# Kernel optimization log

Measured on AMD Instinct MI355X. Metric: run time of the kernel, lower is better.

Reference implementation:

```python
import jax, jax.numpy as jnp
import numpy as np
import math

VOCAB = 390
D = 512
D_INNER = 2048
H = 8
DH = D // H
L = 6
MAX_SEQ = 1024
BATCH = 4
OUT = 2
PAD = 0
EPS = 1e-6


def sinusoid(max_seq, d):
    pos = np.arange(max_seq, dtype=np.float64)[:, None]
    i = np.arange(d, dtype=np.float64)[None, :]
    angle = (pos * np.exp(-np.log(10000.0) * i / d) * np.exp(np.log(10000.0) / d * (i % 2))
             + 0.5 * np.pi * (i % 2))
    return np.sin(angle)[None].astype(np.float32)  # [1, max_seq, d]


def setup_inputs() -> dict:
    key = jax.random.key(0)
    ks = jax.random.split(key, 16)
    s = 0.02
    emb = jax.random.uniform(ks[0], (VOCAB, D), jnp.float32, -0.1, 0.1)
    emb = emb.at[PAD].set(0.0)  # padding_idx row zeroed
    inp = {
        'x': jax.random.randint(ks[1], (BATCH, MAX_SEQ), 0, VOCAB, dtype=jnp.int64) if jax.config.jax_enable_x64 else jax.random.randint(ks[1], (BATCH, MAX_SEQ), 0, VOCAB, dtype=jnp.int32),
        'emb': emb,
        'pos': jnp.asarray(sinusoid(MAX_SEQ, D)),
        'Wq': jax.random.normal(ks[2], (L, D, D), jnp.float32) * s,
        'bq': jnp.zeros((L, D), jnp.float32),
        'Wk': jax.random.normal(ks[3], (L, D, D), jnp.float32) * s,
        'bk': jnp.zeros((L, D), jnp.float32),
        'Wv': jax.random.normal(ks[4], (L, D, D), jnp.float32) * s,
        'bv': jnp.zeros((L, D), jnp.float32),
        'Wo': jax.random.normal(ks[5], (L, D, D), jnp.float32) * s,
        'bo': jnp.zeros((L, D), jnp.float32),
        'E': jax.random.normal(ks[6], (L, MAX_SEQ, DH), jnp.float32),
        'W1': jax.random.normal(ks[7], (L, D, D_INNER), jnp.float32) * s,
        'b1': jnp.zeros((L, D_INNER), jnp.float32),
        'W2': jax.random.normal(ks[8], (L, D_INNER, D), jnp.float32) * s,
        'b2': jnp.zeros((L, D), jnp.float32),
        'ln1_s': jnp.ones((L, D), jnp.float32),
        'ln1_b': jnp.zeros((L, D), jnp.float32),
        'ln2_s': jnp.ones((L, D), jnp.float32),
        'ln2_b': jnp.zeros((L, D), jnp.float32),
        'Wf': jax.random.normal(ks[9], (D, OUT), jnp.float32) * s,
        'bf': jnp.zeros((OUT,), jnp.float32),
    }
    return inp


def _layernorm(x, scale, bias):
    mu = jnp.mean(x, axis=-1, keepdims=True)
    var = jnp.mean(jnp.square(x - mu), axis=-1, keepdims=True)
    return (x - mu) * jax.lax.rsqrt(var + EPS) * scale + bias


def _rel_attention(x, Wq, bq, Wk, bk, Wv, bv, Wo, bo, E):
    b, s, d = x.shape
    q = (x @ Wq + bq).reshape(b, s, H, DH).transpose(0, 2, 1, 3)  # [b,h,s,dh]
    k = (x @ Wk + bk).reshape(b, s, H, DH).transpose(0, 2, 1, 3)
    v = (x @ Wv + bv).reshape(b, s, H, DH).transpose(0, 2, 1, 3)
    m = MAX_SEQ  # len_q == len_k == max_seq -> full E
    QE = jnp.einsum('bhld,md->bhlm', q, E)  # [b,h,s,m]
    # qe masking: keep position j >= m-1-i for query row i
    keep = (jnp.arange(m)[None, :] >= (m - 1 - jnp.arange(s))[:, None]).astype(QE.dtype)
    QE = QE * keep
    # skewing trick: pad-left on last dim, reshape, drop first row
    padded = jnp.pad(QE, ((0, 0), (0, 0), (0, 0), (1, 0)))  # [b,h,s,m+1]
    Srel = padded.reshape(b, H, m + 1, s)[:, :, 1:, :]  # [b,h,m,s] == [b,h,s,s]
    logits = (jnp.einsum('bhqd,bhkd->bhqk', q, k) + Srel) / math.sqrt(DH)
    attn = jax.nn.softmax(logits, axis=-1)
    out = jnp.einsum('bhqk,bhkd->bhqd', attn, v)
    out = out.transpose(0, 2, 1, 3).reshape(b, s, d)
    return out @ Wo + bo


def reference(x, emb, pos, Wq, bq, Wk, bk, Wv, bv, Wo, bo, E, W1, b1, W2, b2,
              ln1_s, ln1_b, ln2_s, ln2_b, Wf, bf):
    h = emb[x] * math.sqrt(D)  # [b,s,d]
    h = h + pos[:, :h.shape[1], :]
    for i in range(L):
        attn = _rel_attention(h, Wq[i], bq[i], Wk[i], bk[i], Wv[i], bv[i], Wo[i], bo[i], E[i])
        h1 = _layernorm(attn + h, ln1_s[i], ln1_b[i])
        ffn = jax.nn.relu(h1 @ W1[i] + b1[i]) @ W2[i] + b2[i]
        h = _layernorm(h1 + ffn, ln2_s[i], ln2_b[i])
    return jnp.tanh(h[:, 0, :] @ Wf + bf)  # [b, OUT]
```

## Files before the change

### kernel.cpp

```cpp
#include <hip/hip_runtime.h>
#include <math.h>

#define BATCH  4
#define SEQ    1024
#define DM     512
#define DI     2048
#define NH     8
#define DH     64
#define NL     6
#define NOUT   2

typedef unsigned short u16;
typedef short s16x8 __attribute__((ext_vector_type(8)));
typedef float f32x4 __attribute__((ext_vector_type(4)));
typedef unsigned short u16x4 __attribute__((ext_vector_type(4)));

#define MFMA16(a, b, c) __builtin_amdgcn_mfma_f32_16x16x32_bf16((a), (b), (c), 0, 0, 0)

static constexpr float SQRT_D = 22.627416997969522f;

__device__ __forceinline__ u16 f2b(float x) {
    union { float f; unsigned u; } v; v.f = x;
    unsigned r = v.u + 0x7fffu + ((v.u >> 16) & 1u);
    return (u16)(r >> 16);
}
__device__ __forceinline__ float b2f(u16 b) {
    union { unsigned u; float f; } v; v.u = ((unsigned)b) << 16; return v.f;
}

__global__ __launch_bounds__(256) void k_embed(const int* __restrict__ x,
                                               const float* __restrict__ emb,
                                               const float* __restrict__ pos,
                                               float* __restrict__ h,
                                               u16* __restrict__ hb) {
    const int idx = blockIdx.x * 256 + threadIdx.x;
    const int d4  = idx & 127;
    const int bs  = idx >> 7;
    const int s   = bs & (SEQ - 1);
    const int tok = x[bs];
    const float4 e = ((const float4*)emb)[tok * 128 + d4];
    const float4 p = ((const float4*)pos)[s * 128 + d4];
    float4 r;
    r.x = e.x * SQRT_D + p.x;  r.y = e.y * SQRT_D + p.y;
    r.z = e.z * SQRT_D + p.z;  r.w = e.w * SQRT_D + p.w;
    ((float4*)h)[idx] = r;
    u16x4 rb = { f2b(r.x), f2b(r.y), f2b(r.z), f2b(r.w) };
    ((u16x4*)hb)[idx] = rb;
}

__global__ __launch_bounds__(256) void k_conv(const float* __restrict__ Wq, const float* __restrict__ Wk,
                                              const float* __restrict__ Wv, const float* __restrict__ Wo,
                                              const float* __restrict__ W1, const float* __restrict__ W2,
                                              const float* __restrict__ E,
                                              u16* __restrict__ Wqkvt, u16* __restrict__ Wot,
                                              u16* __restrict__ W1t,  u16* __restrict__ W2t,
                                              u16* __restrict__ Ebf, int layer) {
    const int tb = blockIdx.x;
    if (tb >= 3072) {
        const int rem = tb - 3072;
        const int idx = rem * 1024 + threadIdx.x * 4;
        const float4 v = *(const float4*)(E + (size_t)layer * SEQ * DH + idx);
        u16x4 o = { f2b(v.x), f2b(v.y), f2b(v.z), f2b(v.w) };
        *(u16x4*)(Ebf + idx) = o;
        return;
    }
    __shared__ float T[32][33];
    const float* src; u16* dst; int Ksz, Nsz, tk, tn;
    if (tb < 768) {
        const int mat = tb >> 8, rem = tb & 255;
        src = (mat == 0 ? Wq : (mat == 1 ? Wk : Wv)) + (size_t)layer * DM * DM;
        dst = Wqkvt + (size_t)mat * DM * DM;
        Ksz = 512; Nsz = 512; tk = rem & 15; tn = rem >> 4;
    } else if (tb < 1024) {
        const int rem = tb - 768;
        src = Wo + (size_t)layer * DM * DM; dst = Wot;
        Ksz = 512; Nsz = 512; tk = rem & 15; tn = rem >> 4;
    } else if (tb < 2048) {
        const int rem = tb - 1024;
        src = W1 + (size_t)layer * DM * DI; dst = W1t;
        Ksz = 512; Nsz = 2048; tk = rem & 15; tn = rem >> 4;
    } else {
        const int rem = tb - 2048;
        src = W2 + (size_t)layer * DI * DM; dst = W2t;
        Ksz = 2048; Nsz = 512; tk = rem >> 4; tn = rem & 15;
    }
    {
        const int rr = threadIdx.x >> 3, c4 = (threadIdx.x & 7) << 2;
        const float4 v = *(const float4*)(src + (size_t)(tk * 32 + rr) * Nsz + tn * 32 + c4);
        T[rr][c4 + 0] = v.x; T[rr][c4 + 1] = v.y; T[rr][c4 + 2] = v.z; T[rr][c4 + 3] = v.w;
    }
    __syncthreads();
    {
        const int nl = threadIdx.x >> 3, k4 = (threadIdx.x & 7) << 2;
        u16x4 o = { f2b(T[k4 + 0][nl]), f2b(T[k4 + 1][nl]), f2b(T[k4 + 2][nl]), f2b(T[k4 + 3][nl]) };
        *(u16x4*)(dst + (size_t)(tn * 32 + nl) * Ksz + tk * 32 + k4) = o;
    }
}

template <int RELU, int WRITE_BF16>
__global__ __launch_bounds__(256) void k_mm(const u16* __restrict__ A,
                                            const u16* __restrict__ Bt,
                                            const float* __restrict__ bias0,
                                            const float* __restrict__ bias1,
                                            const float* __restrict__ bias2,
                                            float* __restrict__ Cf,
                                            u16* __restrict__ Cb,
                                            int K, int ldc, int seg_shift, size_t seg_stride) {
    __shared__ u16 As[128 * 40];
    __shared__ u16 Bs[128 * 40];

    const int n0 = blockIdx.x << 7;
    const int m0 = blockIdx.y << 7;
    const int t  = threadIdx.x;
    const int lane = t & 63, w = t >> 6;
    const int n16 = lane & 15, quad = lane >> 4;
    const int wr = (w & 1) << 6;
    const int wc = (w >> 1) << 6;

    const f32x4 z = {0.f, 0.f, 0.f, 0.f};
    f32x4 acc[4][4];
#pragma unroll
    for (int i = 0; i < 4; ++i)
#pragma unroll
        for (int j = 0; j < 4; ++j) acc[i][j] = z;

    const int sr = t >> 2, sk = (t & 3) << 3;
    const u16* Ag = A  + (size_t)(m0 + sr) * K + sk;
    const u16* Bg = Bt + (size_t)(n0 + sr) * K + sk;

    for (int k0 = 0; k0 < K; k0 += 32) {
        __syncthreads();
        *(uint4*)&As[sr * 40 + sk]        = *(const uint4*)(Ag + k0);
        *(uint4*)&As[(sr + 64) * 40 + sk] = *(const uint4*)(Ag + (size_t)64 * K + k0);
        *(uint4*)&Bs[sr * 40 + sk]        = *(const uint4*)(Bg + k0);
        *(uint4*)&Bs[(sr + 64) * 40 + sk] = *(const uint4*)(Bg + (size_t)64 * K + k0);
        __syncthreads();

        s16x8 af[4], bfr[4];
#pragma unroll
        for (int rb = 0; rb < 4; ++rb)
            af[rb] = *(const s16x8*)&As[(wr + rb * 16 + n16) * 40 + quad * 8];
#pragma unroll
        for (int cb = 0; cb < 4; ++cb)
            bfr[cb] = *(const s16x8*)&Bs[(wc + cb * 16 + n16) * 40 + quad * 8];
#pragma unroll
        for (int rb = 0; rb < 4; ++rb)
#pragma unroll
            for (int cb = 0; cb < 4; ++cb)
                acc[rb][cb] = MFMA16(af[rb], bfr[cb], acc[rb][cb]);
    }

    const int sel = n0 >> seg_shift;
    const int colbase = (n0 & ((1 << seg_shift) - 1)) + wc;
    const float* bias = (sel == 0) ? bias0 : (sel == 1 ? bias1 : bias2);
    const size_t cbase = (size_t)sel * seg_stride;

#pragma unroll
    for (int cb = 0; cb < 4; ++cb) {
        const int col = colbase + cb * 16 + n16;
        const float bv = bias[col];
#pragma unroll
        for (int rb = 0; rb < 4; ++rb) {
#pragma unroll
            for (int rr = 0; rr < 4; ++rr) {
                const int row = m0 + wr + rb * 16 + quad * 4 + rr;
                float v = acc[rb][cb][rr] + bv;
                if (RELU) v = fmaxf(v, 0.f);
                const size_t idx = cbase + (size_t)row * ldc + col;
                if (WRITE_BF16) Cb[idx] = f2b(v);
                else            Cf[idx] = v;
            }
        }
    }
}

__global__ __launch_bounds__(256) void k_attn(const u16* __restrict__ Qg,
                                              const u16* __restrict__ Kg,
                                              const u16* __restrict__ Vg,
                                              const u16* __restrict__ Eg,
                                              u16* __restrict__ Og) {
    __shared__ u16 Qs[64 * 72];
    __shared__ u16 Ks[64 * 72];
    __shared__ u16 Vts[64 * 72];
    __shared__ u16 Ps[64 * 72];
    __shared__ float arena[64 * 128];
    u16* Es = (u16*)arena;

    const int i0 = blockIdx.x << 6;
    const int hd = blockIdx.y;
    const int b  = blockIdx.z;
    const int t  = threadIdx.x;
    const int lane = t & 63;
    const int n16 = lane & 15;
    const int quad = lane >> 4;
    const int w = t >> 6;
    const int rw = w << 4;

    const size_t gb = (size_t)b * SEQ * DM + hd * DH;

    {
        int c = t, r = c >> 3, k8 = (c & 7) << 3;
        *(uint4*)&Qs[r * 72 + k8] = *(const uint4*)(Qg + gb + (size_t)(i0 + r) * DM + k8);
        c = t + 256; r = c >> 3; k8 = (c & 7) << 3;
        *(uint4*)&Qs[r * 72 + k8] = *(const uint4*)(Qg + gb + (size_t)(i0 + r) * DM + k8);
    }

    const f32x4 z = {0.f, 0.f, 0.f, 0.f};
    f32x4 Oa[4] = {z, z, z, z};
    float m_run[4] = {-1e30f, -1e30f, -1e30f, -1e30f};
    float l_run[4] = {0.f, 0.f, 0.f, 0.f};

    for (int ct = 0; ct < 16; ++ct) {
        const int c0 = ct << 6;
        const bool active = (c0 <= i0);

        __syncthreads();
        {
            int c = t, r = c >> 3, k8 = (c & 7) << 3;
            *(uint4*)&Ks[r * 72 + k8] = *(const uint4*)(Kg + gb + (size_t)(c0 + r) * DM + k8);
            c = t + 256; r = c >> 3; k8 = (c & 7) << 3;
            *(uint4*)&Ks[r * 72 + k8] = *(const uint4*)(Kg + gb + (size_t)(c0 + r) * DM + k8);
        }
        {
            int c = t, j = c >> 3, d8 = (c & 7) << 3;
            uint4 v = *(const uint4*)(Vg + gb + (size_t)(c0 + j) * DM + d8);
            const u16* pv = (const u16*)&v;
#pragma unroll
            for (int e = 0; e < 8; ++e) Vts[(d8 + e) * 72 + j] = pv[e];
            c = t + 256; j = c >> 3; d8 = (c & 7) << 3;
            v = *(const uint4*)(Vg + gb + (size_t)(c0 + j) * DM + d8);
            const u16* pv2 = (const u16*)&v;
#pragma unroll
            for (int e = 0; e < 8; ++e) Vts[(d8 + e) * 72 + j] = pv2[e];
        }
        if (active) {
            const int eb = 960 - i0 + c0;
#pragma unroll
            for (int p = 0; p < 4; ++p) {
                const int c = t + (p << 8);
                const int u = c >> 3, k8 = (c & 7) << 3;
                int m = eb + u; m = m > 1023 ? 1023 : m;
                *(uint4*)&Es[u * 72 + k8] = *(const uint4*)(Eg + (size_t)m * DH + k8);
            }
        }
        __syncthreads();

        const s16x8 qa0 = *(const s16x8*)&Qs[(rw + n16) * 72 + quad * 8];
        const s16x8 qa1 = *(const s16x8*)&Qs[(rw + n16) * 72 + quad * 8 + 32];

        f32x4 S[4] = {z, z, z, z};
#pragma unroll
        for (int cb = 0; cb < 4; ++cb) {
            const s16x8 k0 = *(const s16x8*)&Ks[(cb * 16 + n16) * 72 + quad * 8];
            const s16x8 k1 = *(const s16x8*)&Ks[(cb * 16 + n16) * 72 + quad * 8 + 32];
            S[cb] = MFMA16(qa0, k0, S[cb]);
            S[cb] = MFMA16(qa1, k1, S[cb]);
        }

        if (active) {
            f32x4 qe[8];
#pragma unroll
            for (int ub = 0; ub < 8; ++ub) qe[ub] = z;
#pragma unroll
            for (int ub = 0; ub < 8; ++ub) {
                const s16x8 e0 = *(const s16x8*)&Es[(ub * 16 + n16) * 72 + quad * 8];
                const s16x8 e1 = *(const s16x8*)&Es[(ub * 16 + n16) * 72 + quad * 8 + 32];
                qe[ub] = MFMA16(qa0, e0, qe[ub]);
                qe[ub] = MFMA16(qa1, e1, qe[ub]);
            }
            __syncthreads();
#pragma unroll
            for (int ub = 0; ub < 8; ++ub)
#pragma unroll
                for (int rr = 0; rr < 4; ++rr)
                    arena[(rw + quad * 4 + rr) * 128 + ub * 16 + n16] = qe[ub][rr];
            const int dqc = i0 - c0;
#pragma unroll
            for (int cb = 0; cb < 4; ++cb)
#pragma unroll
                for (int rr = 0; rr < 4; ++rr) {
                    const int ir = rw + quad * 4 + rr;
                    const int d = cb * 16 + n16 - ir;
                    const float srel = (d <= dqc) ? arena[ir * 128 + 63 + d] : 0.f;
                    S[cb][rr] = (S[cb][rr] + srel) * 0.125f;
                }
        } else {
#pragma unroll
            for (int cb = 0; cb < 4; ++cb)
#pragma unroll
                for (int rr = 0; rr < 4; ++rr) S[cb][rr] *= 0.125f;
        }

        float mt[4], al[4], rs[4], p[4][4];
#pragma unroll
        for (int rr = 0; rr < 4; ++rr)
            mt[rr] = fmaxf(fmaxf(S[0][rr], S[1][rr]), fmaxf(S[2][rr], S[3][rr]));
#pragma unroll
        for (int rr = 0; rr < 4; ++rr) {
            mt[rr] = fmaxf(mt[rr], __shfl_xor(mt[rr], 1, 64));
            mt[rr] = fmaxf(mt[rr], __shfl_xor(mt[rr], 2, 64));
            mt[rr] = fmaxf(mt[rr], __shfl_xor(mt[rr], 4, 64));
            mt[rr] = fmaxf(mt[rr], __shfl_xor(mt[rr], 8, 64));
        }
#pragma unroll
        for (int rr = 0; rr < 4; ++rr) {
            const float mn = fmaxf(m_run[rr], mt[rr]);
            al[rr] = __expf(m_run[rr] - mn);
            m_run[rr] = mn;
        }
#pragma unroll
        for (int cb = 0; cb < 4; ++cb)
#pragma unroll
            for (int rr = 0; rr < 4; ++rr) p[cb][rr] = __expf(S[cb][rr] - m_run[rr]);
#pragma unroll
        for (int rr = 0; rr < 4; ++rr) {
            rs[rr] = p[0][rr] + p[1][rr] + p[2][rr] + p[3][rr];
            rs[rr] += __shfl_xor(rs[rr], 1, 64);
            rs[rr] += __shfl_xor(rs[rr], 2, 64);
            rs[rr] += __shfl_xor(rs[rr], 4, 64);
            rs[rr] += __shfl_xor(rs[rr], 8, 64);
            l_run[rr] = l_run[rr] * al[rr] + rs[rr];
        }
#pragma unroll
        for (int db = 0; db < 4; ++db)
#pragma unroll
            for (int rr = 0; rr < 4; ++rr) Oa[db][rr] *= al[rr];
#pragma unroll
        for (int cb = 0; cb < 4; ++cb)
#pragma unroll
            for (int rr = 0; rr < 4; ++rr)
                Ps[(rw + quad * 4 + rr) * 72 + cb * 16 + n16] = f2b(p[cb][rr]);

        const s16x8 pa0 = *(const s16x8*)&Ps[(rw + n16) * 72 + quad * 8];
        const s16x8 pa1 = *(const s16x8*)&Ps[(rw + n16) * 72 + quad * 8 + 32];
#pragma unroll
        for (int db = 0; db < 4; ++db) {
            const s16x8 v0 = *(const s16x8*)&Vts[(db * 16 + n16) * 72 + quad * 8];
            const s16x8 v1 = *(const s16x8*)&Vts[(db * 16 + n16) * 72 + quad * 8 + 32];
            Oa[db] = MFMA16(pa0, v0, Oa[db]);
            Oa[db] = MFMA16(pa1, v1, Oa[db]);
        }
    }

    float inv[4];
#pragma unroll
    for (int rr = 0; rr < 4; ++rr) inv[rr] = 1.f / l_run[rr];
#pragma unroll
    for (int db = 0; db < 4; ++db)
#pragma unroll
        for (int rr = 0; rr < 4; ++rr) {
            const int row = i0 + rw + quad * 4 + rr;
            Og[gb + (size_t)row * DM + db * 16 + n16] = f2b(Oa[db][rr] * inv[rr]);
        }
}

__global__ __launch_bounds__(128) void k_ln(const float* __restrict__ A,
                                            const float* __restrict__ R,
                                            const float* __restrict__ sc,
                                            const float* __restrict__ bi,
                                            float* __restrict__ Y,
                                            u16* __restrict__ Yb) {
    const int r = blockIdx.x, t = threadIdx.x;
    const float4 a = ((const float4*)(A + (size_t)r * DM))[t];
    const float4 b = ((const float4*)(R + (size_t)r * DM))[t];
    float4 v;
    v.x = a.x + b.x; v.y = a.y + b.y; v.z = a.z + b.z; v.w = a.w + b.w;

    float s = v.x + v.y + v.z + v.w;
#pragma unroll
    for (int o = 32; o > 0; o >>= 1) s += __shfl_down(s, o, 64);
    __shared__ float r1[2], r2[2];
    if ((t & 63) == 0) r1[t >> 6] = s;
    __syncthreads();
    const float mean = (r1[0] + r1[1]) * (1.f / 512.f);

    float4 d;
    d.x = v.x - mean; d.y = v.y - mean; d.z = v.z - mean; d.w = v.w - mean;
    float q = d.x * d.x + d.y * d.y + d.z * d.z + d.w * d.w;
#pragma unroll
    for (int o = 32; o > 0; o >>= 1) q += __shfl_down(q, o, 64);
    if ((t & 63) == 0) r2[t >> 6] = q;
    __syncthreads();
    const float rsq = rsqrtf((r2[0] + r2[1]) * (1.f / 512.f) + 1e-6f);

    const float4 s4 = ((const float4*)sc)[t];
    const float4 b4 = ((const float4*)bi)[t];
    float4 y;
    y.x = d.x * rsq * s4.x + b4.x;
    y.y = d.y * rsq * s4.y + b4.y;
    y.z = d.z * rsq * s4.z + b4.z;
    y.w = d.w * rsq * s4.w + b4.w;
    ((float4*)(Y + (size_t)r * DM))[t] = y;
    u16x4 yb = { f2b(y.x), f2b(y.y), f2b(y.z), f2b(y.w) };
    ((u16x4*)(Yb + (size_t)r * DM))[t] = yb;
}

__global__ __launch_bounds__(512) void k_head(const float* __restrict__ h,
                                              const float* __restrict__ Wf,
                                              const float* __restrict__ bf,
                                              float* __restrict__ out) {
    const int t = threadIdx.x;
    const int w = t >> 6, lane = t & 63;
    const int b = w >> 1, oo = w & 1;
    float s = 0.f;
    for (int d = lane; d < DM; d += 64)
        s += h[(size_t)b * SEQ * DM + d] * Wf[d * NOUT + oo];
#pragma unroll
    for (int o = 32; o > 0; o >>= 1) s += __shfl_down(s, o, 64);
    if (lane == 0) out[b * NOUT + oo] = tanhf(s + bf[oo]);
}

extern "C" void kernel_launch(void* const* d_in, const int* in_sizes, int n_in,
                              void* d_out, int out_size, void* d_ws, size_t ws_size,
                              hipStream_t stream) {
    const int*   x    = (const int*)d_in[0];
    const float* emb  = (const float*)d_in[1];
    const float* pos  = (const float*)d_in[2];
    const float* Wq   = (const float*)d_in[3];
    const float* bq   = (const float*)d_in[4];
    const float* Wk   = (const float*)d_in[5];
    const float* bk   = (const float*)d_in[6];
    const float* Wv   = (const float*)d_in[7];
    const float* bv   = (const float*)d_in[8];
    const float* Wo   = (const float*)d_in[9];
    const float* bo   = (const float*)d_in[10];
    const float* E    = (const float*)d_in[11];
    const float* W1   = (const float*)d_in[12];
    const float* b1   = (const float*)d_in[13];
    const float* W2   = (const float*)d_in[14];
    const float* b2   = (const float*)d_in[15];
    const float* ln1s = (const float*)d_in[16];
    const float* ln1b = (const float*)d_in[17];
    const float* ln2s = (const float*)d_in[18];
    const float* ln2b = (const float*)d_in[19];
    const float* Wf   = (const float*)d_in[20];
    const float* bfp  = (const float*)d_in[21];
    float* out = (float*)d_out;

    char* W = (char*)d_ws;
    float* h    = (float*)(W);
    float* h1   = (float*)(W + (8u  << 20));
    u16*   hb   = (u16*)  (W + (16u << 20));
    u16*   h1b  = (u16*)  (W + (20u << 20));
    u16*   qb   = (u16*)  (W + (24u << 20));
    u16*   kb   = (u16*)  (W + (28u << 20));
    u16*   vb   = (u16*)  (W + (32u << 20));
    u16*   tb   = (u16*)  (W + (36u << 20));
    u16*   midb = qb;
    u16*   Wqkvt= (u16*)  (W + (40u << 20));
    u16*   Wot  = (u16*)  (W + (40u << 20) + 1572864);
    u16*   W1t  = (u16*)  (W + (42u << 20));
    u16*   W2t  = (u16*)  (W + (44u << 20));
    u16*   Ebf  = (u16*)  (W + (46u << 20));

    const int M = BATCH * SEQ;
    const size_t SEG = (size_t)M * DM;

    k_embed<<<(BATCH * SEQ * DM / 4) / 256, 256, 0, stream>>>(x, emb, pos, h, hb);

    for (int l = 0; l < NL; ++l) {
        k_conv<<<3136, 256, 0, stream>>>(Wq, Wk, Wv, Wo, W1, W2, E,
                                         Wqkvt, Wot, W1t, W2t, Ebf, l);
        k_mm<0, 1><<<dim3(12, 32), 256, 0, stream>>>(hb, Wqkvt,
            bq + l * DM, bk + l * DM, bv + l * DM, nullptr, qb, 512, 512, 9, SEG);
        k_attn<<<dim3(16, 8, 4), 256, 0, stream>>>(qb, kb, vb, Ebf, tb);
        k_mm<0, 0><<<dim3(4, 32), 256, 0, stream>>>(tb, Wot,
            bo + l * DM, bo + l * DM, bo + l * DM, h1, nullptr, 512, 512, 30, 0);
        k_ln<<<M, 128, 0, stream>>>(h1, h, ln1s + l * DM, ln1b + l * DM, h1, h1b);
        k_mm<1, 1><<<dim3(16, 32), 256, 0, stream>>>(h1b, W1t,
            b1 + l * DI, b1 + l * DI, b1 + l * DI, nullptr, midb, 512, 2048, 30, 0);
        k_mm<0, 0><<<dim3(4, 32), 256, 0, stream>>>(midb, W2t,
            b2 + l * DM, b2 + l * DM, b2 + l * DM, h, nullptr, 2048, 512, 30, 0);
        k_ln<<<M, 128, 0, stream>>>(h, h1, ln2s + l * DM, ln2b + l * DM, h, hb);
    }

    k_head<<<1, 512, 0, stream>>>(h, Wf, bfp, out);
}
```

Measured before the change: 1.248 ms.

## Batch weight conversion, write V transposed from GEMM, restructure attention and LayerNorm

```diff
diff --git a/kernel.cpp b/kernel.cpp
--- a/kernel.cpp
+++ b/kernel.cpp
@@ -18,6 +18,12 @@
 #define MFMA16(a, b, c) __builtin_amdgcn_mfma_f32_16x16x32_bf16((a), (b), (c), 0, 0, 0)
 
 static constexpr float SQRT_D = 22.627416997969522f;
+
+#define SLOT_WO   786432
+#define SLOT_W1   1048576
+#define SLOT_W2   2097152
+#define SLOT_E    3145728
+#define SLOT_SZ   3211264
 
 __device__ __forceinline__ u16 f2b(float x) {
     union { float f; unsigned u; } v; v.f = x;
@@ -52,10 +58,16 @@
                                               const float* __restrict__ Wv, const float* __restrict__ Wo,
                                               const float* __restrict__ W1, const float* __restrict__ W2,
                                               const float* __restrict__ E,
-                                              u16* __restrict__ Wqkvt, u16* __restrict__ Wot,
-                                              u16* __restrict__ W1t,  u16* __restrict__ W2t,
-                                              u16* __restrict__ Ebf, int layer) {
-    const int tb = blockIdx.x;
+                                              u16* __restrict__ wbase, int layer0, int slot_stride) {
+    const int ll = blockIdx.x / 3136;
+    const int tb = blockIdx.x - ll * 3136;
+    const int layer = layer0 + ll;
+    u16* Wqkvt = wbase + (size_t)ll * slot_stride;
+    u16* Wot   = Wqkvt + SLOT_WO;
+    u16* W1t   = Wqkvt + SLOT_W1;
+    u16* W2t   = Wqkvt + SLOT_W2;
+    u16* Ebf   = Wqkvt + SLOT_E;
+
     if (tb >= 3072) {
         const int rem = tb - 3072;
         const int idx = rem * 1024 + threadIdx.x * 4;
@@ -97,7 +109,7 @@
     }
 }
 
-template <int RELU, int WRITE_BF16>
+template <int RELU, int WRITE_BF16, int SEGV>
 __global__ __launch_bounds__(256) void k_mm(const u16* __restrict__ A,
                                             const u16* __restrict__ Bt,
                                             const float* __restrict__ bias0,
@@ -105,6 +117,7 @@
                                             const float* __restrict__ bias2,
                                             float* __restrict__ Cf,
                                             u16* __restrict__ Cb,
+                                            u16* __restrict__ Vt,
                                             int K, int ldc, int seg_shift, size_t seg_stride) {
     __shared__ u16 As[128 * 40];
     __shared__ u16 Bs[128 * 40];
@@ -166,9 +179,15 @@
                 const int row = m0 + wr + rb * 16 + quad * 4 + rr;
                 float v = acc[rb][cb][rr] + bv;
                 if (RELU) v = fmaxf(v, 0.f);
-                const size_t idx = cbase + (size_t)row * ldc + col;
-                if (WRITE_BF16) Cb[idx] = f2b(v);
-                else            Cf[idx] = v;
+                if (SEGV && sel == 2) {
+                    const size_t vi = (((size_t)(row >> 10) * NH + (col >> 6)) * DH + (col & 63))
+                                      * SEQ + (row & (SEQ - 1));
+                    Vt[vi] = f2b(v);
+                } else if (WRITE_BF16) {
+                    Cb[cbase + (size_t)row * ldc + col] = f2b(v);
+                } else {
+                    Cf[cbase + (size_t)row * ldc + col] = v;
+                }
             }
         }
     }
@@ -176,15 +195,11 @@
 
 __global__ __launch_bounds__(256) void k_attn(const u16* __restrict__ Qg,
                                               const u16* __restrict__ Kg,
-                                              const u16* __restrict__ Vg,
+                                              const u16* __restrict__ Vt,
                                               const u16* __restrict__ Eg,
                                               u16* __restrict__ Og) {
-    __shared__ u16 Qs[64 * 72];
-    __shared__ u16 Ks[64 * 72];
-    __shared__ u16 Vts[64 * 72];
+    __shared__ u16 arena[128 * 72];
     __shared__ u16 Ps[64 * 72];
-    __shared__ float arena[64 * 128];
-    u16* Es = (u16*)arena;
 
     const int i0 = blockIdx.x << 6;
     const int hd = blockIdx.y;
@@ -193,95 +208,65 @@
     const int lane = t & 63;
     const int n16 = lane & 15;
     const int quad = lane >> 4;
-    const int w = t >> 6;
-    const int rw = w << 4;
-
-    const size_t gb = (size_t)b * SEQ * DM + hd * DH;
-
-    {
-        int c = t, r = c >> 3, k8 = (c & 7) << 3;
-        *(uint4*)&Qs[r * 72 + k8] = *(const uint4*)(Qg + gb + (size_t)(i0 + r) * DM + k8);
-        c = t + 256; r = c >> 3; k8 = (c & 7) << 3;
-        *(uint4*)&Qs[r * 72 + k8] = *(const uint4*)(Qg + gb + (size_t)(i0 + r) * DM + k8);
-    }
+    const int rw = (t >> 6) << 4;
+    const int ir_base = rw + (quad << 2);
+
+    const size_t gb  = (size_t)b * SEQ * DM + hd * DH;
+    const size_t vtb = ((size_t)b * NH + hd) * DH * SEQ;
+
+    const u16* qp = Qg + gb + (size_t)(i0 + rw + n16) * DM + quad * 8;
+    const s16x8 qa0 = *(const s16x8*)qp;
+    const s16x8 qa1 = *(const s16x8*)(qp + 32);
 
     const f32x4 z = {0.f, 0.f, 0.f, 0.f};
     f32x4 Oa[4] = {z, z, z, z};
-    float m_run[4] = {-1e30f, -1e30f, -1e30f, -1e30f};
     float l_run[4] = {0.f, 0.f, 0.f, 0.f};
 
     for (int ct = 0; ct < 16; ++ct) {
         const int c0 = ct << 6;
-        const bool active = (c0 <= i0);
-
-        __syncthreads();
-        {
-            int c = t, r = c >> 3, k8 = (c & 7) << 3;
-            *(uint4*)&Ks[r * 72 + k8] = *(const uint4*)(Kg + gb + (size_t)(c0 + r) * DM + k8);
-            c = t + 256; r = c >> 3; k8 = (c & 7) << 3;
-            *(uint4*)&Ks[r * 72 + k8] = *(const uint4*)(Kg + gb + (size_t)(c0 + r) * DM + k8);
-        }
-        {
-            int c = t, j = c >> 3, d8 = (c & 7) << 3;
-            uint4 v = *(const uint4*)(Vg + gb + (size_t)(c0 + j) * DM + d8);
-            const u16* pv = (const u16*)&v;
-#pragma unroll
-            for (int e = 0; e < 8; ++e) Vts[(d8 + e) * 72 + j] = pv[e];
-            c = t + 256; j = c >> 3; d8 = (c & 7) << 3;
-            v = *(const uint4*)(Vg + gb + (size_t)(c0 + j) * DM + d8);
-            const u16* pv2 = (const u16*)&v;
-#pragma unroll
-            for (int e = 0; e < 8; ++e) Vts[(d8 + e) * 72 + j] = pv2[e];
-        }
-        if (active) {
+
+        f32x4 S[4];
+#pragma unroll
+        for (int cb = 0; cb < 4; ++cb) {
+            const u16* kp = Kg + gb + (size_t)(c0 + cb * 16 + n16) * DM + quad * 8;
+            S[cb] = MFMA16(qa0, *(const s16x8*)kp, z);
+            S[cb] = MFMA16(qa1, *(const s16x8*)(kp + 32), S[cb]);
+        }
+
+        if (c0 <= i0) {
             const int eb = 960 - i0 + c0;
-#pragma unroll
-            for (int p = 0; p < 4; ++p) {
-                const int c = t + (p << 8);
-                const int u = c >> 3, k8 = (c & 7) << 3;
-                int m = eb + u; m = m > 1023 ? 1023 : m;
-                *(uint4*)&Es[u * 72 + k8] = *(const uint4*)(Eg + (size_t)m * DH + k8);
+            if (ct == 0) {
+#pragma unroll
+                for (int ub = 0; ub < 8; ++ub) {
+                    int er = eb + ub * 16 + n16; er = er > 1023 ? 1023 : er;
+                    const u16* ep = Eg + er * DH;
+                    f32x4 qe = MFMA16(qa0, *(const s16x8*)ep, z);
+                    qe = MFMA16(qa1, *(const s16x8*)(ep + 32), qe);
+                    u16x4 qpk = { f2b(qe[0]), f2b(qe[1]), f2b(qe[2]), f2b(qe[3]) };
+                    *(u16x4*)&arena[(ub * 16 + n16) * 72 + ir_base] = qpk;
+                }
+            } else {
+                const int pbase = ((ct + 1) & 1) << 6;
+#pragma unroll
+                for (int ub = 0; ub < 4; ++ub) {
+                    int er = eb + 64 + ub * 16 + n16; er = er > 1023 ? 1023 : er;
+                    const u16* ep = Eg + er * DH;
+                    f32x4 qe = MFMA16(qa0, *(const s16x8*)ep, z);
+                    qe = MFMA16(qa1, *(const s16x8*)(ep + 32), qe);
+                    u16x4 qpk = { f2b(qe[0]), f2b(qe[1]), f2b(qe[2]), f2b(qe[3]) };
+                    *(u16x4*)&arena[(pbase + ub * 16 + n16) * 72 + ir_base] = qpk;
+                }
             }
-        }
-        __syncthreads();
-
-        const s16x8 qa0 = *(const s16x8*)&Qs[(rw + n16) * 72 + quad * 8];
-        const s16x8 qa1 = *(const s16x8*)&Qs[(rw + n16) * 72 + quad * 8 + 32];
-
-        f32x4 S[4] = {z, z, z, z};
-#pragma unroll
-        for (int cb = 0; cb < 4; ++cb) {
-            const s16x8 k0 = *(const s16x8*)&Ks[(cb * 16 + n16) * 72 + quad * 8];
-            const s16x8 k1 = *(const s16x8*)&Ks[(cb * 16 + n16) * 72 + quad * 8 + 32];
-            S[cb] = MFMA16(qa0, k0, S[cb]);
-            S[cb] = MFMA16(qa1, k1, S[cb]);
-        }
-
-        if (active) {
-            f32x4 qe[8];
-#pragma unroll
-            for (int ub = 0; ub < 8; ++ub) qe[ub] = z;
-#pragma unroll
-            for (int ub = 0; ub < 8; ++ub) {
-                const s16x8 e0 = *(const s16x8*)&Es[(ub * 16 + n16) * 72 + quad * 8];
-                const s16x8 e1 = *(const s16x8*)&Es[(ub * 16 + n16) * 72 + quad * 8 + 32];
-                qe[ub] = MFMA16(qa0, e0, qe[ub]);
-                qe[ub] = MFMA16(qa1, e1, qe[ub]);
-            }
-            __syncthreads();
-#pragma unroll
-            for (int ub = 0; ub < 8; ++ub)
-#pragma unroll
-                for (int rr = 0; rr < 4; ++rr)
-                    arena[(rw + quad * 4 + rr) * 128 + ub * 16 + n16] = qe[ub][rr];
             const int dqc = i0 - c0;
+            const int rot = ct << 6;
 #pragma unroll
             for (int cb = 0; cb < 4; ++cb)
 #pragma unroll
                 for (int rr = 0; rr < 4; ++rr) {
-                    const int ir = rw + quad * 4 + rr;
+                    const int ir = ir_base + rr;
                     const int d = cb * 16 + n16 - ir;
-                    const float srel = (d <= dqc) ? arena[ir * 128 + 63 + d] : 0.f;
+                    const float srel = (d <= dqc)
+                        ? b2f(arena[((63 + d + rot) & 127) * 72 + ir]) : 0.f;
                     S[cb][rr] = (S[cb][rr] + srel) * 0.125f;
                 }
         } else {
@@ -291,76 +276,58 @@
                 for (int rr = 0; rr < 4; ++rr) S[cb][rr] *= 0.125f;
         }
 
-        float mt[4], al[4], rs[4], p[4][4];
-#pragma unroll
-        for (int rr = 0; rr < 4; ++rr)
-            mt[rr] = fmaxf(fmaxf(S[0][rr], S[1][rr]), fmaxf(S[2][rr], S[3][rr]));
+        float p[4][4];
+#pragma unroll
+        for (int cb = 0; cb < 4; ++cb)
+#pragma unroll
+            for (int rr = 0; rr < 4; ++rr) p[cb][rr] = __expf(S[cb][rr]);
 #pragma unroll
         for (int rr = 0; rr < 4; ++rr) {
-            mt[rr] = fmaxf(mt[rr], __shfl_xor(mt[rr], 1, 64));
-            mt[rr] = fmaxf(mt[rr], __shfl_xor(mt[rr], 2, 64));
-            mt[rr] = fmaxf(mt[rr], __shfl_xor(mt[rr], 4, 64));
-            mt[rr] = fmaxf(mt[rr], __shfl_xor(mt[rr], 8, 64));
-        }
-#pragma unroll
-        for (int rr = 0; rr < 4; ++rr) {
-            const float mn = fmaxf(m_run[rr], mt[rr]);
-            al[rr] = __expf(m_run[rr] - mn);
-            m_run[rr] = mn;
-        }
+            float rs = p[0][rr] + p[1][rr] + p[2][rr] + p[3][rr];
+            rs += __shfl_xor(rs, 1, 64);
+            rs += __shfl_xor(rs, 2, 64);
+            rs += __shfl_xor(rs, 4, 64);
+            rs += __shfl_xor(rs, 8, 64);
+            l_run[rr] += rs;
+        }
+
 #pragma unroll
         for (int cb = 0; cb < 4; ++cb)
 #pragma unroll
-            for (int rr = 0; rr < 4; ++rr) p[cb][rr] = __expf(S[cb][rr] - m_run[rr]);
-#pragma unroll
-        for (int rr = 0; rr < 4; ++rr) {
-            rs[rr] = p[0][rr] + p[1][rr] + p[2][rr] + p[3][rr];
-            rs[rr] += __shfl_xor(rs[rr], 1, 64);
-            rs[rr] += __shfl_xor(rs[rr], 2, 64);
-            rs[rr] += __shfl_xor(rs[rr], 4, 64);
-            rs[rr] += __shfl_xor(rs[rr], 8, 64);
-            l_run[rr] = l_run[rr] * al[rr] + rs[rr];
-        }
-#pragma unroll
-        for (int db = 0; db < 4; ++db)
-#pragma unroll
-            for (int rr = 0; rr < 4; ++rr) Oa[db][rr] *= al[rr];
-#pragma unroll
-        for (int cb = 0; cb < 4; ++cb)
-#pragma unroll
             for (int rr = 0; rr < 4; ++rr)
-                Ps[(rw + quad * 4 + rr) * 72 + cb * 16 + n16] = f2b(p[cb][rr]);
+                Ps[(ir_base + rr) * 72 + cb * 16 + n16] = f2b(p[cb][rr]);
 
         const s16x8 pa0 = *(const s16x8*)&Ps[(rw + n16) * 72 + quad * 8];
         const s16x8 pa1 = *(const s16x8*)&Ps[(rw + n16) * 72 + quad * 8 + 32];
 #pragma unroll
         for (int db = 0; db < 4; ++db) {
-            const s16x8 v0 = *(const s16x8*)&Vts[(db * 16 + n16) * 72 + quad * 8];
-            const s16x8 v1 = *(const s16x8*)&Vts[(db * 16 + n16) * 72 + quad * 8 + 32];
-            Oa[db] = MFMA16(pa0, v0, Oa[db]);
-            Oa[db] = MFMA16(pa1, v1, Oa[db]);
-        }
-    }
-
-    float inv[4];
-#pragma unroll
-    for (int rr = 0; rr < 4; ++rr) inv[rr] = 1.f / l_run[rr];
+            const u16* vp = Vt + vtb + (size_t)(db * 16 + n16) * SEQ + c0 + quad * 8;
+            Oa[db] = MFMA16(pa0, *(const s16x8*)vp, Oa[db]);
+            Oa[db] = MFMA16(pa1, *(const s16x8*)(vp + 32), Oa[db]);
+        }
+    }
+
+#pragma unroll
+    for (int rr = 0; rr < 4; ++rr) l_run[rr] = 1.f / l_run[rr];
 #pragma unroll
     for (int db = 0; db < 4; ++db)
 #pragma unroll
         for (int rr = 0; rr < 4; ++rr) {
-            const int row = i0 + rw + quad * 4 + rr;
-            Og[gb + (size_t)row * DM + db * 16 + n16] = f2b(Oa[db][rr] * inv[rr]);
-        }
-}
-
-__global__ __launch_bounds__(128) void k_ln(const float* __restrict__ A,
+            const int row = i0 + ir_base + rr;
+            Og[gb + (size_t)row * DM + db * 16 + n16] = f2b(Oa[db][rr] * l_run[rr]);
+        }
+}
+
+__global__ __launch_bounds__(256) void k_ln(const float* __restrict__ A,
                                             const float* __restrict__ R,
                                             const float* __restrict__ sc,
                                             const float* __restrict__ bi,
                                             float* __restrict__ Y,
                                             u16* __restrict__ Yb) {
-    const int r = blockIdx.x, t = threadIdx.x;
+    const int g = threadIdx.x >> 7;
+    const int r = (blockIdx.x << 1) + g;
+    const int t = threadIdx.x & 127;
+    const int w = threadIdx.x >> 6;
     const float4 a = ((const float4*)(A + (size_t)r * DM))[t];
     const float4 b = ((const float4*)(R + (size_t)r * DM))[t];
     float4 v;
@@ -369,19 +336,19 @@
     float s = v.x + v.y + v.z + v.w;
 #pragma unroll
     for (int o = 32; o > 0; o >>= 1) s += __shfl_down(s, o, 64);
-    __shared__ float r1[2], r2[2];
-    if ((t & 63) == 0) r1[t >> 6] = s;
+    __shared__ float r1[4], r2[4];
+    if ((threadIdx.x & 63) == 0) r1[w] = s;
     __syncthreads();
-    const float mean = (r1[0] + r1[1]) * (1.f / 512.f);
+    const float mean = (r1[g << 1] + r1[(g << 1) + 1]) * (1.f / 512.f);
 
     float4 d;
     d.x = v.x - mean; d.y = v.y - mean; d.z = v.z - mean; d.w = v.w - mean;
     float q = d.x * d.x + d.y * d.y + d.z * d.z + d.w * d.w;
 #pragma unroll
     for (int o = 32; o > 0; o >>= 1) q += __shfl_down(q, o, 64);
-    if ((t & 63) == 0) r2[t >> 6] = q;
+    if ((threadIdx.x & 63) == 0) r2[w] = q;
     __syncthreads();
-    const float rsq = rsqrtf((r2[0] + r2[1]) * (1.f / 512.f) + 1e-6f);
+    const float rsq = rsqrtf((r2[g << 1] + r2[(g << 1) + 1]) * (1.f / 512.f) + 1e-6f);
 
     const float4 s4 = ((const float4*)sc)[t];
     const float4 b4 = ((const float4*)bi)[t];
@@ -444,34 +411,42 @@
     u16*   h1b  = (u16*)  (W + (20u << 20));
     u16*   qb   = (u16*)  (W + (24u << 20));
     u16*   kb   = (u16*)  (W + (28u << 20));
-    u16*   vb   = (u16*)  (W + (32u << 20));
+    u16*   Vt   = (u16*)  (W + (32u << 20));
     u16*   tb   = (u16*)  (W + (36u << 20));
     u16*   midb = qb;
-    u16*   Wqkvt= (u16*)  (W + (40u << 20));
-    u16*   Wot  = (u16*)  (W + (40u << 20) + 1572864);
-    u16*   W1t  = (u16*)  (W + (42u << 20));
-    u16*   W2t  = (u16*)  (W + (44u << 20));
-    u16*   Ebf  = (u16*)  (W + (46u << 20));
+    u16*   Wb   = (u16*)  (W + (40u << 20));
+    (void)kb;
+
+    const bool all = ws_size >= (size_t)80478208ull;
 
     const int M = BATCH * SEQ;
     const size_t SEG = (size_t)M * DM;
 
     k_embed<<<(BATCH * SEQ * DM / 4) / 256, 256, 0, stream>>>(x, emb, pos, h, hb);
+    if (all)
+        k_conv<<<6 * 3136, 256, 0, stream>>>(Wq, Wk, Wv, Wo, W1, W2, E, Wb, 0, SLOT_SZ);
 
     for (int l = 0; l < NL; ++l) {
-        k_conv<<<3136, 256, 0, stream>>>(Wq, Wk, Wv, Wo, W1, W2, E,
-                                         Wqkvt, Wot, W1t, W2t, Ebf, l);
-        k_mm<0, 1><<<dim3(12, 32), 256, 0, stream>>>(hb, Wqkvt,
-            bq + l * DM, bk + l * DM, bv + l * DM, nullptr, qb, 512, 512, 9, SEG);
-        k_attn<<<dim3(16, 8, 4), 256, 0, stream>>>(qb, kb, vb, Ebf, tb);
-        k_mm<0, 0><<<dim3(4, 32), 256, 0, stream>>>(tb, Wot,
-            bo + l * DM, bo + l * DM, bo + l * DM, h1, nullptr, 512, 512, 30, 0);
-        k_ln<<<M, 128, 0, stream>>>(h1, h, ln1s + l * DM, ln1b + l * DM, h1, h1b);
-        k_mm<1, 1><<<dim3(16, 32), 256, 0, stream>>>(h1b, W1t,
-            b1 + l * DI, b1 + l * DI, b1 + l * DI, nullptr, midb, 512, 2048, 30, 0);
-        k_mm<0, 0><<<dim3(4, 32), 256, 0, stream>>>(midb, W2t,
-            b2 + l * DM, b2 + l * DM, b2 + l * DM, h, nullptr, 2048, 512, 30, 0);
-        k_ln<<<M, 128, 0, stream>>>(h, h1, ln2s + l * DM, ln2b + l * DM, h, hb);
+        if (!all)
+            k_conv<<<3136, 256, 0, stream>>>(Wq, Wk, Wv, Wo, W1, W2, E, Wb, l, 0);
+        u16* wl   = Wb + (size_t)(all ? l : 0) * SLOT_SZ;
+        u16* wqkv = wl;
+        u16* wot  = wl + SLOT_WO;
+        u16* w1t  = wl + SLOT_W1;
+        u16* w2t  = wl + SLOT_W2;
+        u16* ebf  = wl + SLOT_E;
+
+        k_mm<0, 1, 1><<<dim3(12, 32), 256, 0, stream>>>(hb, wqkv,
+            bq + l * DM, bk + l * DM, bv + l * DM, nullptr, qb, Vt, 512, 512, 9, SEG);
+        k_attn<<<dim3(16, 8, 4), 256, 0, stream>>>(qb, kb, Vt, ebf, tb);
+        k_mm<0, 0, 0><<<dim3(4, 32), 256, 0, stream>>>(tb, wot,
+            bo + l * DM, bo + l * DM, bo + l * DM, h1, nullptr, nullptr, 512, 512, 30, 0);
+        k_ln<<<M / 2, 256, 0, stream>>>(h1, h, ln1s + l * DM, ln1b + l * DM, h1, h1b);
+        k_mm<1, 1, 0><<<dim3(16, 32), 256, 0, stream>>>(h1b, w1t,
+            b1 + l * DI, b1 + l * DI, b1 + l * DI, nullptr, midb, nullptr, 512, 2048, 30, 0);
+        k_mm<0, 0, 0><<<dim3(4, 32), 256, 0, stream>>>(midb, w2t,
+            b2 + l * DM, b2 + l * DM, b2 + l * DM, h, nullptr, nullptr, 2048, 512, 30, 0);
+        k_ln<<<M / 2, 256, 0, stream>>>(h, h1, ln2s + l * DM, ln2b + l * DM, h, hb);
     }
 
     k_head<<<1, 512, 0, stream>>>(h, Wf, bfp, out);
```

Measured after the change: 1.488 ms. 1.19x slower.
